# Kernel tuning notes

Measured on AMD Instinct MI355X. Metric: run time of the kernel, lower is better.

## Reference

```python
import jax, jax.numpy as jnp
import numpy as np

N = 100000      # nodes
D_IN = 512      # in_size
D_OUT = 512     # out_size
E = 200000      # edges per etype
EPS = 1e-5      # LayerNorm eps


def setup_inputs() -> dict:
    key = jax.random.key(0)
    ks = jax.random.split(key, 10)
    scale = 1.0 / np.sqrt(D_IN)
    inp = {
        "x": jax.random.normal(ks[0], (N, D_IN), jnp.float32),
        "W0": jax.random.normal(ks[1], (D_OUT, D_IN), jnp.float32) * scale,
        "W1": jax.random.normal(ks[2], (D_OUT, D_IN), jnp.float32) * scale,
        "W2": jax.random.normal(ks[3], (D_OUT, D_IN), jnp.float32) * scale,
        "gamma": jnp.ones((D_OUT,), jnp.float32),
        "beta": jnp.zeros((D_OUT,), jnp.float32),
        "src0": jax.random.randint(ks[4], (E,), 0, N, jnp.int32),
        "dst0": jax.random.randint(ks[5], (E,), 0, N, jnp.int32),
        "src1": jax.random.randint(ks[6], (E,), 0, N, jnp.int32),
        "dst1": jax.random.randint(ks[7], (E,), 0, N, jnp.int32),
        "src2": jax.random.randint(ks[8], (E,), 0, N, jnp.int32),
        "dst2": jax.random.randint(ks[9], (E,), 0, N, jnp.int32),
    }
    return inp


def _segment_mean(msgs, dst, n):
    # per-dst-node mean; 0 for nodes with no incoming edges (DGL fn.mean semantics)
    s = jax.ops.segment_sum(msgs, dst, num_segments=n)
    c = jax.ops.segment_sum(jnp.ones((msgs.shape[0],), msgs.dtype), dst, num_segments=n)
    return s / jnp.maximum(c, 1.0)[:, None]


def reference(x, W0, W1, W2, gamma, beta, src0, dst0, src1, dst1, src2, dst2):
    # relation-specific linear transforms, averaged over etypes sharing the src ntype
    h = (x @ W0.T + x @ W1.T + x @ W2.T) / 3.0            # [N, D_OUT]
    # per-etype copy_u / mean aggregation
    a0 = _segment_mean(h[src0], dst0, N)
    a1 = _segment_mean(h[src1], dst1, N)
    a2 = _segment_mean(h[src2], dst2, N)
    # cross-etype 'mean' reducer
    h_agg = (a0 + a1 + a2) / 3.0
    # LayerNorm(ReLU(h_agg))
    a = jax.nn.relu(h_agg)
    mu = jnp.mean(a, axis=-1, keepdims=True)
    var = jnp.mean(jnp.square(a - mu), axis=-1, keepdims=True)
    return (a - mu) * jax.lax.rsqrt(var + EPS) * gamma + beta
```

## Files before the change

kernel.cpp:

```cpp
#include <hip/hip_runtime.h>
#include <hip/hip_bf16.h>
#include <cstdint>
#include <cstddef>

#define N_NODES 100000
#define DIM 512
#define NE 200000
#define NBLK 391

typedef __attribute__((ext_vector_type(4))) float floatx4;
typedef __attribute__((ext_vector_type(8))) short shortx8;

__device__ __forceinline__ unsigned short f2bf(float f) {
    union { float f; uint32_t u; } v; v.f = f;
    uint32_t r = v.u + 0x7fff + ((v.u >> 16) & 1);
    return (unsigned short)(r >> 16);
}

__device__ __forceinline__ float bf2f(unsigned short h) {
    union { uint32_t u; float f; } v; v.u = ((uint32_t)h) << 16;
    return v.f;
}

__device__ __forceinline__ shortx8 cvt8(const float4 a, const float4 b) {
    union { __hip_bfloat162 h2[4]; shortx8 s8; } u;
    u.h2[0] = __float22bfloat162_rn(make_float2(a.x, a.y));
    u.h2[1] = __float22bfloat162_rn(make_float2(a.z, a.w));
    u.h2[2] = __float22bfloat162_rn(make_float2(b.x, b.y));
    u.h2[3] = __float22bfloat162_rn(make_float2(b.z, b.w));
    return u.s8;
}

__device__ __forceinline__ void load_lds16(const void* g, void* l) {
    __builtin_amdgcn_global_load_lds(
        (const __attribute__((address_space(1))) uint32_t*)g,
        (__attribute__((address_space(3))) uint32_t*)l, 16, 0, 0);
}

__global__ __launch_bounds__(256) void combine_w_kernel(
    const float* __restrict__ W0, const float* __restrict__ W1,
    const float* __restrict__ W2, unsigned short* __restrict__ Wc) {
    int i = blockIdx.x * 256 + threadIdx.x;
    Wc[i] = f2bf((W0[i] + W1[i] + W2[i]) * (1.0f / 3.0f));
}

__global__ __launch_bounds__(256) void count_kernel(
    const int* __restrict__ d0, const int* __restrict__ d1,
    const int* __restrict__ d2, int* __restrict__ cnt) {
    int t = blockIdx.x * 256 + threadIdx.x;
    if (t >= 3 * NE) return;
    int e = t / NE;
    int i = t - e * NE;
    const int* dp = (e == 0) ? d0 : (e == 1) ? d1 : d2;
    atomicAdd(&cnt[e * N_NODES + dp[i]], 1);
}

__global__ __launch_bounds__(256) void scan1_kernel(
    const int* __restrict__ cnt, int* __restrict__ bsum) {
    int t = threadIdx.x;
    int n = blockIdx.x * 256 + t;
    int rl = 0;
    if (n < N_NODES) rl = cnt[n] + cnt[N_NODES + n] + cnt[2 * N_NODES + n];
    int v = rl;
    #pragma unroll
    for (int off = 32; off > 0; off >>= 1) v += __shfl_xor(v, off);
    __shared__ int ws_[4];
    if ((t & 63) == 0) ws_[t >> 6] = v;
    __syncthreads();
    if (t == 0) bsum[blockIdx.x] = ws_[0] + ws_[1] + ws_[2] + ws_[3];
}

__global__ __launch_bounds__(512) void scan2_kernel(
    const int* __restrict__ bsum, int* __restrict__ boff) {
    __shared__ int sh[512];
    int t = threadIdx.x;
    int v = (t < NBLK) ? bsum[t] : 0;
    sh[t] = v;
    __syncthreads();
    #pragma unroll
    for (int off = 1; off < 512; off <<= 1) {
        int add = (t >= off) ? sh[t - off] : 0;
        __syncthreads();
        sh[t] += add;
        __syncthreads();
    }
    if (t < NBLK) boff[t] = sh[t] - v;
}

__global__ __launch_bounds__(256) void scan3_kernel(
    const int* __restrict__ cnt, const int* __restrict__ boff,
    int* __restrict__ row_start, int* __restrict__ cursor) {
    __shared__ int sh[256];
    int t = threadIdx.x;
    int n = blockIdx.x * 256 + t;
    int rl = 0;
    if (n < N_NODES) rl = cnt[n] + cnt[N_NODES + n] + cnt[2 * N_NODES + n];
    sh[t] = rl;
    __syncthreads();
    #pragma unroll
    for (int off = 1; off < 256; off <<= 1) {
        int add = (t >= off) ? sh[t - off] : 0;
        __syncthreads();
        sh[t] += add;
        __syncthreads();
    }
    if (n < N_NODES) {
        int excl = sh[t] - rl + boff[blockIdx.x];
        row_start[n] = excl;
        cursor[n] = excl;
    }
}

__global__ __launch_bounds__(256) void bin_kernel(
    const int* __restrict__ s0, const int* __restrict__ d0,
    const int* __restrict__ s1, const int* __restrict__ d1,
    const int* __restrict__ s2, const int* __restrict__ d2,
    int* __restrict__ cursor, int* __restrict__ src_tag) {
    int t = blockIdx.x * 256 + threadIdx.x;
    if (t >= 3 * NE) return;
    int e = t / NE;
    int i = t - e * NE;
    const int* sp; const int* dp;
    if (e == 0)      { sp = s0; dp = d0; }
    else if (e == 1) { sp = s1; dp = d1; }
    else             { sp = s2; dp = d2; }
    int d = dp[i];
    int pos = atomicAdd(&cursor[d], 1);
    src_tag[pos] = sp[i] | (e << 30);
}

__global__ __launch_bounds__(256) void gemm_kernel(
    const float* __restrict__ X, const unsigned short* __restrict__ B,
    unsigned short* __restrict__ H, int M) {
    __shared__ alignas(16) unsigned short As[128 * 64];
    __shared__ alignas(16) unsigned short Bs[128 * 64];
    const int tid = threadIdx.x;
    const int lane = tid & 63;
    const int w = tid >> 6;
    const int wr = w >> 1, wc = w & 1;
    const int q = lane >> 4, r = lane & 15;

    int lid = ((int)blockIdx.x & 7) * 391 + ((int)blockIdx.x >> 3);
    int mt = lid >> 2, nt = lid & 3;
    int m0 = mt * 128, n0 = nt * 128;

    const float* aptr[4];
    #pragma unroll
    for (int i = 0; i < 4; ++i) {
        int ca = i * 256 + tid;
        int row = ca & 127, c = ca >> 7;
        int gm = m0 + row; if (gm >= M) gm = M - 1;
        aptr[i] = X + (size_t)gm * DIM + c * 8;
    }
    float4 areg[4][2];
    auto aload = [&](int k0_) {
        #pragma unroll
        for (int i = 0; i < 4; ++i) {
            areg[i][0] = *(const float4*)(aptr[i] + k0_);
            areg[i][1] = *(const float4*)(aptr[i] + k0_ + 4);
        }
    };

    floatx4 acc[4][4] = {};
    aload(0);

    for (int k0 = 0; k0 < DIM; k0 += 64) {
        #pragma unroll
        for (int i = 0; i < 4; ++i) {
            int cb = i * 256 + tid;
            int row = cb & 127, c = cb >> 7;
            load_lds16(&B[(size_t)(n0 + row) * DIM + k0 + c * 8], &Bs[cb * 8]);
        }
        #pragma unroll
        for (int i = 0; i < 4; ++i)
            *(shortx8*)&As[(i * 256 + tid) * 8] = cvt8(areg[i][0], areg[i][1]);
        __syncthreads();
        if (k0 + 64 < DIM) aload(k0 + 64);

        #pragma unroll
        for (int kk = 0; kk < 2; ++kk) {
            shortx8 af[4], bfr[4];
            #pragma unroll
            for (int mi = 0; mi < 4; ++mi)
                af[mi] = *(const shortx8*)&As[((kk * 4 + q) * 128 + wr * 64 + mi * 16 + r) * 8];
            #pragma unroll
            for (int nj = 0; nj < 4; ++nj)
                bfr[nj] = *(const shortx8*)&Bs[((kk * 4 + q) * 128 + wc * 64 + nj * 16 + r) * 8];
            #pragma unroll
            for (int mi = 0; mi < 4; ++mi)
                #pragma unroll
                for (int nj = 0; nj < 4; ++nj)
                    acc[mi][nj] = __builtin_amdgcn_mfma_f32_16x16x32_bf16(
                        af[mi], bfr[nj], acc[mi][nj], 0, 0, 0);
        }
        __syncthreads();
    }

    #pragma unroll
    for (int mi = 0; mi < 4; ++mi) {
        #pragma unroll
        for (int rg = 0; rg < 4; ++rg) {
            int gm = m0 + wr * 64 + mi * 16 + q * 4 + rg;
            if (gm < M) {
                #pragma unroll
                for (int nj = 0; nj < 4; ++nj)
                    H[(size_t)gm * DIM + n0 + wc * 64 + nj * 16 + r] =
                        f2bf(acc[mi][nj][rg]);
            }
        }
    }
}

__global__ __launch_bounds__(256) void gather_ln_kernel(
    const unsigned short* __restrict__ h, const int* __restrict__ row_start,
    const int* __restrict__ cnt, const int* __restrict__ src_tag,
    const float* __restrict__ gamma, const float* __restrict__ beta,
    float* __restrict__ out) {
    const int lane = threadIdx.x & 63;
    const int n = blockIdx.x * 4 + (threadIdx.x >> 6);
    if (n >= N_NODES) return;
    const int c0 = cnt[n], c1 = cnt[N_NODES + n], c2 = cnt[2 * N_NODES + n];
    const int len = c0 + c1 + c2;
    const float w0 = 1.0f / (3.0f * (float)max(c0, 1));
    const float w1 = 1.0f / (3.0f * (float)max(c1, 1));
    const float w2 = 1.0f / (3.0f * (float)max(c2, 1));
    const int beg = row_start[n];
    const size_t lx = (size_t)lane * 8;
    float acc[8] = {};
    for (int base = 0; base < len; base += 64) {
        int rem = len - base;
        int m = rem < 64 ? rem : 64;
        int tag = (lane < m) ? src_tag[beg + base + lane] : 0;
        int j = 0;
        for (; j + 4 <= m; j += 4) {
            int u0 = __shfl(tag, j),     u1 = __shfl(tag, j + 1);
            int u2 = __shfl(tag, j + 2), u3 = __shfl(tag, j + 3);
            int e0 = ((unsigned)u0) >> 30, e1 = ((unsigned)u1) >> 30;
            int e2 = ((unsigned)u2) >> 30, e3 = ((unsigned)u3) >> 30;
            float g0 = (e0 == 0) ? w0 : ((e0 == 1) ? w1 : w2);
            float g1 = (e1 == 0) ? w0 : ((e1 == 1) ? w1 : w2);
            float g2 = (e2 == 0) ? w0 : ((e2 == 1) ? w1 : w2);
            float g3 = (e3 == 0) ? w0 : ((e3 == 1) ? w1 : w2);
            shortx8 v0 = *(const shortx8*)(h + (size_t)(u0 & 0x3FFFFFFF) * DIM + lx);
            shortx8 v1 = *(const shortx8*)(h + (size_t)(u1 & 0x3FFFFFFF) * DIM + lx);
            shortx8 v2 = *(const shortx8*)(h + (size_t)(u2 & 0x3FFFFFFF) * DIM + lx);
            shortx8 v3 = *(const shortx8*)(h + (size_t)(u3 & 0x3FFFFFFF) * DIM + lx);
            #pragma unroll
            for (int k = 0; k < 8; ++k) {
                acc[k] += bf2f((unsigned short)v0[k]) * g0;
                acc[k] += bf2f((unsigned short)v1[k]) * g1;
                acc[k] += bf2f((unsigned short)v2[k]) * g2;
                acc[k] += bf2f((unsigned short)v3[k]) * g3;
            }
        }
        for (; j < m; ++j) {
            int u = __shfl(tag, j);
            int e = ((unsigned)u) >> 30;
            float wg = (e == 0) ? w0 : ((e == 1) ? w1 : w2);
            shortx8 v = *(const shortx8*)(h + (size_t)(u & 0x3FFFFFFF) * DIM + lx);
            #pragma unroll
            for (int k = 0; k < 8; ++k)
                acc[k] += bf2f((unsigned short)v[k]) * wg;
        }
    }
    float s1_ = 0.0f, s2_ = 0.0f;
    #pragma unroll
    for (int k = 0; k < 8; ++k) {
        float v = fmaxf(acc[k], 0.0f);
        acc[k] = v; s1_ += v; s2_ += v * v;
    }
    #pragma unroll
    for (int off = 1; off < 64; off <<= 1) {
        s1_ += __shfl_xor(s1_, off);
        s2_ += __shfl_xor(s2_, off);
    }
    float mu = s1_ * (1.0f / DIM);
    float var = s2_ * (1.0f / DIM) - mu * mu;
    float rstd = rsqrtf(var + 1e-5f);
    float4 g0 = *(const float4*)(gamma + lane * 8);
    float4 g1 = *(const float4*)(gamma + lane * 8 + 4);
    float4 b0 = *(const float4*)(beta + lane * 8);
    float4 b1 = *(const float4*)(beta + lane * 8 + 4);
    float4 o0, o1;
    o0.x = (acc[0] - mu) * rstd * g0.x + b0.x;
    o0.y = (acc[1] - mu) * rstd * g0.y + b0.y;
    o0.z = (acc[2] - mu) * rstd * g0.z + b0.z;
    o0.w = (acc[3] - mu) * rstd * g0.w + b0.w;
    o1.x = (acc[4] - mu) * rstd * g1.x + b1.x;
    o1.y = (acc[5] - mu) * rstd * g1.y + b1.y;
    o1.z = (acc[6] - mu) * rstd * g1.z + b1.z;
    o1.w = (acc[7] - mu) * rstd * g1.w + b1.w;
    float4* op = (float4*)(out + (size_t)n * DIM + lane * 8);
    op[0] = o0;
    op[1] = o1;
}

extern "C" void kernel_launch(void* const* d_in, const int* in_sizes, int n_in,
                              void* d_out, int out_size, void* d_ws, size_t ws_size,
                              hipStream_t stream) {
    const float* x     = (const float*)d_in[0];
    const float* W0    = (const float*)d_in[1];
    const float* W1    = (const float*)d_in[2];
    const float* W2    = (const float*)d_in[3];
    const float* gamma = (const float*)d_in[4];
    const float* beta  = (const float*)d_in[5];
    const int* s0  = (const int*)d_in[6];
    const int* dd0 = (const int*)d_in[7];
    const int* s1  = (const int*)d_in[8];
    const int* dd1 = (const int*)d_in[9];
    const int* s2  = (const int*)d_in[10];
    const int* dd2 = (const int*)d_in[11];
    float* out = (float*)d_out;

    char* ws = (char*)d_ws;
    size_t off = 0;
    int* cnt = (int*)(ws + off);             off += 3u * N_NODES * 4u;
    int* row_start = (int*)(ws + off);       off += (size_t)N_NODES * 4u;
    int* cursor = (int*)(ws + off);          off += (size_t)N_NODES * 4u;
    int* bsum = (int*)(ws + off);            off += 2048;
    int* boff = (int*)(ws + off);            off += 2048;
    int* src_tag = (int*)(ws + off);         off += (size_t)3 * NE * 4u;
    unsigned short* Wc = (unsigned short*)(ws + off); off += (size_t)DIM * DIM * 2u;
    off = (off + 255) & ~255ull;
    unsigned short* h = (unsigned short*)(ws + off);

    hipMemsetAsync(cnt, 0, (size_t)3 * N_NODES * sizeof(int), stream);

    combine_w_kernel<<<(DIM * DIM) / 256, 256, 0, stream>>>(W0, W1, W2, Wc);
    count_kernel<<<(3 * NE + 255) / 256, 256, 0, stream>>>(dd0, dd1, dd2, cnt);
    scan1_kernel<<<NBLK, 256, 0, stream>>>(cnt, bsum);
    scan2_kernel<<<1, 512, 0, stream>>>(bsum, boff);
    scan3_kernel<<<NBLK, 256, 0, stream>>>(cnt, boff, row_start, cursor);
    bin_kernel<<<(3 * NE + 255) / 256, 256, 0, stream>>>(
        s0, dd0, s1, dd1, s2, dd2, cursor, src_tag);

    gemm_kernel<<<3128, 256, 0, stream>>>(x, Wc, h, N_NODES);

    gather_ln_kernel<<<(N_NODES + 3) / 4, 256, 0, stream>>>(
        h, row_start, cnt, src_tag, gamma, beta, out);
}
```

Baseline: 632.4 us.

## Make GEMM persistent with resident swizzled weight tile and merge preprocessing kernels

The GEMM becomes a persistent kernel of 256 blocks with 512 threads. Each block loads its whole 128x512 bf16 slice of the combined weight into LDS once, using an XOR swizzle to avoid bank conflicts. It then loops over 256-row tiles of x, double-buffering the fp32 loads in registers with a k-step of 32. Separately, the weight-combine and edge-count kernels are fused into one launch, and the single-block scan2 is folded into scan3 so each block rescans the block sums itself. The aim is to cut weight reloads and launch overhead. In exchange the GEMM now runs one large-LDS block per CU, syncs twice per short k-step, and has uneven tile counts across blocks.

```diff
diff --git a/kernel.cpp b/kernel.cpp
--- a/kernel.cpp
+++ b/kernel.cpp
@@ -6,7 +6,8 @@
 #define N_NODES 100000
 #define DIM 512
 #define NE 200000
-#define NBLK 391
+#define NSB 196
+#define NMT 391
 
 typedef __attribute__((ext_vector_type(4))) float floatx4;
 typedef __attribute__((ext_vector_type(8))) short shortx8;
@@ -37,45 +38,61 @@
         (__attribute__((address_space(3))) uint32_t*)l, 16, 0, 0);
 }
 
-__global__ __launch_bounds__(256) void combine_w_kernel(
+__global__ __launch_bounds__(256) void count_combine_kernel(
+    const int* __restrict__ d0, const int* __restrict__ d1,
+    const int* __restrict__ d2, int* __restrict__ cnt,
     const float* __restrict__ W0, const float* __restrict__ W1,
     const float* __restrict__ W2, unsigned short* __restrict__ Wc) {
-    int i = blockIdx.x * 256 + threadIdx.x;
-    Wc[i] = f2bf((W0[i] + W1[i] + W2[i]) * (1.0f / 3.0f));
-}
-
-__global__ __launch_bounds__(256) void count_kernel(
-    const int* __restrict__ d0, const int* __restrict__ d1,
-    const int* __restrict__ d2, int* __restrict__ cnt) {
     int t = blockIdx.x * 256 + threadIdx.x;
-    if (t >= 3 * NE) return;
-    int e = t / NE;
-    int i = t - e * NE;
-    const int* dp = (e == 0) ? d0 : (e == 1) ? d1 : d2;
-    atomicAdd(&cnt[e * N_NODES + dp[i]], 1);
-}
-
-__global__ __launch_bounds__(256) void scan1_kernel(
+    if (t < DIM * DIM)
+        Wc[t] = f2bf((W0[t] + W1[t] + W2[t]) * (1.0f / 3.0f));
+    if (t < 3 * NE) {
+        int e = t / NE;
+        int i = t - e * NE;
+        const int* dp = (e == 0) ? d0 : (e == 1) ? d1 : d2;
+        atomicAdd(&cnt[e * N_NODES + dp[i]], 1);
+    }
+}
+
+__global__ __launch_bounds__(512) void scan1_kernel(
     const int* __restrict__ cnt, int* __restrict__ bsum) {
     int t = threadIdx.x;
-    int n = blockIdx.x * 256 + t;
+    int n = blockIdx.x * 512 + t;
     int rl = 0;
     if (n < N_NODES) rl = cnt[n] + cnt[N_NODES + n] + cnt[2 * N_NODES + n];
     int v = rl;
     #pragma unroll
     for (int off = 32; off > 0; off >>= 1) v += __shfl_xor(v, off);
-    __shared__ int ws_[4];
+    __shared__ int ws_[8];
     if ((t & 63) == 0) ws_[t >> 6] = v;
     __syncthreads();
-    if (t == 0) bsum[blockIdx.x] = ws_[0] + ws_[1] + ws_[2] + ws_[3];
-}
-
-__global__ __launch_bounds__(512) void scan2_kernel(
-    const int* __restrict__ bsum, int* __restrict__ boff) {
+    if (t == 0) {
+        int s = 0;
+        #pragma unroll
+        for (int i = 0; i < 8; ++i) s += ws_[i];
+        bsum[blockIdx.x] = s;
+    }
+}
+
+__global__ __launch_bounds__(512) void scan3_kernel(
+    const int* __restrict__ cnt, const int* __restrict__ bsum,
+    int* __restrict__ row_start, int* __restrict__ cursor) {
+    __shared__ int shb[512];
     __shared__ int sh[512];
     int t = threadIdx.x;
-    int v = (t < NBLK) ? bsum[t] : 0;
-    sh[t] = v;
+    shb[t] = (t < NSB) ? bsum[t] : 0;
+    __syncthreads();
+    #pragma unroll
+    for (int off = 1; off < 512; off <<= 1) {
+        int add = (t >= off) ? shb[t - off] : 0;
+        __syncthreads();
+        shb[t] += add;
+        __syncthreads();
+    }
+    int n = blockIdx.x * 512 + t;
+    int rl = 0;
+    if (n < N_NODES) rl = cnt[n] + cnt[N_NODES + n] + cnt[2 * N_NODES + n];
+    sh[t] = rl;
     __syncthreads();
     #pragma unroll
     for (int off = 1; off < 512; off <<= 1) {
@@ -84,28 +101,9 @@
         sh[t] += add;
         __syncthreads();
     }
-    if (t < NBLK) boff[t] = sh[t] - v;
-}
-
-__global__ __launch_bounds__(256) void scan3_kernel(
-    const int* __restrict__ cnt, const int* __restrict__ boff,
-    int* __restrict__ row_start, int* __restrict__ cursor) {
-    __shared__ int sh[256];
-    int t = threadIdx.x;
-    int n = blockIdx.x * 256 + t;
-    int rl = 0;
-    if (n < N_NODES) rl = cnt[n] + cnt[N_NODES + n] + cnt[2 * N_NODES + n];
-    sh[t] = rl;
-    __syncthreads();
-    #pragma unroll
-    for (int off = 1; off < 256; off <<= 1) {
-        int add = (t >= off) ? sh[t - off] : 0;
-        __syncthreads();
-        sh[t] += add;
-        __syncthreads();
-    }
     if (n < N_NODES) {
-        int excl = sh[t] - rl + boff[blockIdx.x];
+        int bexcl = shb[blockIdx.x] - bsum[blockIdx.x];
+        int excl = sh[t] - rl + bexcl;
         row_start[n] = excl;
         cursor[n] = excl;
     }
@@ -129,83 +127,100 @@
     src_tag[pos] = sp[i] | (e << 30);
 }
 
-__global__ __launch_bounds__(256) void gemm_kernel(
+__global__ __launch_bounds__(512) void gemm_kernel(
     const float* __restrict__ X, const unsigned short* __restrict__ B,
     unsigned short* __restrict__ H, int M) {
-    __shared__ alignas(16) unsigned short As[128 * 64];
-    __shared__ alignas(16) unsigned short Bs[128 * 64];
+    __shared__ alignas(16) unsigned short Bs[128 * 512];
+    __shared__ alignas(16) unsigned short As[256 * 32];
     const int tid = threadIdx.x;
     const int lane = tid & 63;
     const int w = tid >> 6;
     const int wr = w >> 1, wc = w & 1;
     const int q = lane >> 4, r = lane & 15;
 
-    int lid = ((int)blockIdx.x & 7) * 391 + ((int)blockIdx.x >> 3);
-    int mt = lid >> 2, nt = lid & 3;
-    int m0 = mt * 128, n0 = nt * 128;
-
-    const float* aptr[4];
-    #pragma unroll
-    for (int i = 0; i < 4; ++i) {
-        int ca = i * 256 + tid;
-        int row = ca & 127, c = ca >> 7;
-        int gm = m0 + row; if (gm >= M) gm = M - 1;
-        aptr[i] = X + (size_t)gm * DIM + c * 8;
-    }
-    float4 areg[4][2];
-    auto aload = [&](int k0_) {
-        #pragma unroll
-        for (int i = 0; i < 4; ++i) {
-            areg[i][0] = *(const float4*)(aptr[i] + k0_);
-            areg[i][1] = *(const float4*)(aptr[i] + k0_ + 4);
-        }
-    };
-
-    floatx4 acc[4][4] = {};
-    aload(0);
-
-    for (int k0 = 0; k0 < DIM; k0 += 64) {
-        #pragma unroll
-        for (int i = 0; i < 4; ++i) {
-            int cb = i * 256 + tid;
-            int row = cb & 127, c = cb >> 7;
-            load_lds16(&B[(size_t)(n0 + row) * DIM + k0 + c * 8], &Bs[cb * 8]);
-        }
-        #pragma unroll
-        for (int i = 0; i < 4; ++i)
-            *(shortx8*)&As[(i * 256 + tid) * 8] = cvt8(areg[i][0], areg[i][1]);
-        __syncthreads();
-        if (k0 + 64 < DIM) aload(k0 + 64);
-
-        #pragma unroll
-        for (int kk = 0; kk < 2; ++kk) {
-            shortx8 af[4], bfr[4];
-            #pragma unroll
-            for (int mi = 0; mi < 4; ++mi)
-                af[mi] = *(const shortx8*)&As[((kk * 4 + q) * 128 + wr * 64 + mi * 16 + r) * 8];
-            #pragma unroll
-            for (int nj = 0; nj < 4; ++nj)
-                bfr[nj] = *(const shortx8*)&Bs[((kk * 4 + q) * 128 + wc * 64 + nj * 16 + r) * 8];
+    const int lid = ((int)blockIdx.x & 7) * 32 + ((int)blockIdx.x >> 3);
+    const int nt = lid & 3, mg = lid >> 2;
+    const int n0 = nt * 128;
+
+    #pragma unroll
+    for (int i = 0; i < 16; ++i) {
+        int ch = i * 512 + tid;
+        int row = ch >> 6, c = ch & 63;
+        int cs = c ^ (row & 7);
+        load_lds16(&B[(size_t)(n0 + row) * DIM + cs * 8], &Bs[ch * 8]);
+    }
+
+    for (int mt = mg; mt < NMT; mt += 64) {
+        const int m0 = mt * 256;
+        const float* ap[2];
+        unsigned abyte[2];
+        #pragma unroll
+        for (int i = 0; i < 2; ++i) {
+            int row = i * 128 + (tid >> 2);
+            int c = tid & 3;
+            int cs = c ^ ((row >> 1) & 3);
+            abyte[i] = (unsigned)row * 64 + (unsigned)cs * 16;
+            int gm = m0 + row; if (gm >= M) gm = M - 1;
+            ap[i] = X + (size_t)gm * DIM + c * 8;
+        }
+        float4 SL[2][2][2];
+        #pragma unroll
+        for (int p = 0; p < 2; ++p)
+            #pragma unroll
+            for (int i = 0; i < 2; ++i) {
+                SL[p][i][0] = *(const float4*)(ap[i] + p * 32);
+                SL[p][i][1] = *(const float4*)(ap[i] + p * 32 + 4);
+            }
+
+        floatx4 acc[4][4] = {};
+        #pragma unroll
+        for (int s = 0; s < 16; ++s) {
+            #pragma unroll
+            for (int i = 0; i < 2; ++i)
+                *(shortx8*)((char*)As + abyte[i]) =
+                    cvt8(SL[s & 1][i][0], SL[s & 1][i][1]);
+            if (s + 2 < 16) {
+                #pragma unroll
+                for (int i = 0; i < 2; ++i) {
+                    SL[s & 1][i][0] = *(const float4*)(ap[i] + (s + 2) * 32);
+                    SL[s & 1][i][1] = *(const float4*)(ap[i] + (s + 2) * 32 + 4);
+                }
+            }
+            __syncthreads();
+
+            shortx8 af[4], bf[4];
+            #pragma unroll
+            for (int mi = 0; mi < 4; ++mi) {
+                int m = wr * 64 + mi * 16 + r;
+                af[mi] = *(const shortx8*)((const char*)As +
+                         m * 64 + ((q ^ ((m >> 1) & 3)) << 4));
+            }
+            #pragma unroll
+            for (int nj = 0; nj < 4; ++nj) {
+                int n = wc * 64 + nj * 16 + r;
+                bf[nj] = *(const shortx8*)((const char*)Bs +
+                         n * 1024 + (((4 * s + q) ^ (n & 7)) << 4));
+            }
             #pragma unroll
             for (int mi = 0; mi < 4; ++mi)
                 #pragma unroll
                 for (int nj = 0; nj < 4; ++nj)
                     acc[mi][nj] = __builtin_amdgcn_mfma_f32_16x16x32_bf16(
-                        af[mi], bfr[nj], acc[mi][nj], 0, 0, 0);
-        }
-        __syncthreads();
-    }
-
-    #pragma unroll
-    for (int mi = 0; mi < 4; ++mi) {
-        #pragma unroll
-        for (int rg = 0; rg < 4; ++rg) {
-            int gm = m0 + wr * 64 + mi * 16 + q * 4 + rg;
-            if (gm < M) {
-                #pragma unroll
-                for (int nj = 0; nj < 4; ++nj)
-                    H[(size_t)gm * DIM + n0 + wc * 64 + nj * 16 + r] =
-                        f2bf(acc[mi][nj][rg]);
+                        af[mi], bf[nj], acc[mi][nj], 0, 0, 0);
+            __syncthreads();
+        }
+
+        #pragma unroll
+        for (int mi = 0; mi < 4; ++mi) {
+            #pragma unroll
+            for (int rg = 0; rg < 4; ++rg) {
+                int gm = m0 + wr * 64 + mi * 16 + q * 4 + rg;
+                if (gm < M) {
+                    #pragma unroll
+                    for (int nj = 0; nj < 4; ++nj)
+                        H[(size_t)gm * DIM + n0 + wc * 64 + nj * 16 + r] =
+                            f2bf(acc[mi][nj][rg]);
+                }
             }
         }
     }
@@ -318,7 +333,6 @@
     int* row_start = (int*)(ws + off);       off += (size_t)N_NODES * 4u;
     int* cursor = (int*)(ws + off);          off += (size_t)N_NODES * 4u;
     int* bsum = (int*)(ws + off);            off += 2048;
-    int* boff = (int*)(ws + off);            off += 2048;
     int* src_tag = (int*)(ws + off);         off += (size_t)3 * NE * 4u;
     unsigned short* Wc = (unsigned short*)(ws + off); off += (size_t)DIM * DIM * 2u;
     off = (off + 255) & ~255ull;
@@ -326,15 +340,14 @@
 
     hipMemsetAsync(cnt, 0, (size_t)3 * N_NODES * sizeof(int), stream);
 
-    combine_w_kernel<<<(DIM * DIM) / 256, 256, 0, stream>>>(W0, W1, W2, Wc);
-    count_kernel<<<(3 * NE + 255) / 256, 256, 0, stream>>>(dd0, dd1, dd2, cnt);
-    scan1_kernel<<<NBLK, 256, 0, stream>>>(cnt, bsum);
-    scan2_kernel<<<1, 512, 0, stream>>>(bsum, boff);
-    scan3_kernel<<<NBLK, 256, 0, stream>>>(cnt, boff, row_start, cursor);
+    count_combine_kernel<<<(3 * NE + 255) / 256, 256, 0, stream>>>(
+        dd0, dd1, dd2, cnt, W0, W1, W2, Wc);
+    scan1_kernel<<<NSB, 512, 0, stream>>>(cnt, bsum);
+    scan3_kernel<<<NSB, 512, 0, stream>>>(cnt, bsum, row_start, cursor);
     bin_kernel<<<(3 * NE + 255) / 256, 256, 0, stream>>>(
         s0, dd0, s1, dd1, s2, dd2, cursor, src_tag);
 
-    gemm_kernel<<<3128, 256, 0, stream>>>(x, Wc, h, N_NODES);
+    gemm_kernel<<<256, 512, 0, stream>>>(x, Wc, h, N_NODES);
 
     gather_ln_kernel<<<(N_NODES + 3) / 4, 256, 0, stream>>>(
         h, row_start, cnt, src_tag, gamma, beta, out);
```

After: 594.9 us. 1.06x faster.
